# Performance work log

Measured on AMD Instinct MI355X. Metric: run time of the kernel, lower is better.

Reference implementation:

```python
import jax, jax.numpy as jnp
import numpy as np

EPS = 1e-5
SLOPE = 0.01  # torch LeakyReLU default negative slope


def _bn(h, gamma, beta):
    # BatchNorm1d in training mode: biased batch statistics over the batch dim
    mu = jnp.mean(h, axis=0)
    var = jnp.var(h, axis=0)
    return gamma * (h - mu) * jax.lax.rsqrt(var + EPS) + beta


def _leaky(h):
    return jnp.where(h >= 0, h, SLOPE * h)


def _forward(x, adj, w_gc1, b_gc1, w_gc2, b_gc2, w_gc3, b_gc3,
             w_fc0, b_fc0, g_fc0, be_fc0, w_fc1, b_fc1, g_fc1, be_fc1, w_fc2, b_fc2):
    B, S, Fp1 = x.shape
    F = Fp1 - 1
    N = adj.shape[0]
    # --- scatter: build per-sample node features from first S-1 timesteps ---
    sids = x[:, :S - 1, -2].astype(jnp.int32)                                   # [B,S-1]
    feats = jnp.concatenate([x[:, :S - 1, :-2], x[:, :S - 1, -1:]], axis=-1)    # [B,S-1,F]
    X = jnp.zeros((B, N, F), x.dtype).at[jnp.arange(B)[:, None], sids].set(feats)
    # --- symmetric-normalized adjacency with self loops: D^-1/2 (A+I) D^-1/2 ---
    A = adj + jnp.eye(N, dtype=adj.dtype)
    d = jax.lax.rsqrt(jnp.sum(A, axis=1))
    Ahat = d[:, None] * A * d[None, :]                                          # [N,N]
    # --- fc0 branch on last-timestep features ---
    h0 = _leaky(_bn(x[:, -1, :-2] @ w_fc0 + b_fc0, g_fc0, be_fc0))              # [B,FH]
    # --- 3-layer GCN: relu(Ahat @ X @ W + b) ---
    X = jax.nn.relu(jnp.einsum('mn,bnf->bmf', Ahat, X) @ w_gc1 + b_gc1)
    X = jax.nn.relu(jnp.einsum('mn,bnf->bmf', Ahat, X) @ w_gc2 + b_gc2)
    X = jax.nn.relu(jnp.einsum('mn,bnf->bmf', Ahat, X) @ w_gc3 + b_gc3)         # [B,N,GH]
    # --- gather station-specific rows ---
    sid_last = x[:, -1, -2].astype(jnp.int32)                                   # [B]
    g = X[jnp.arange(B), sid_last]                                              # [B,GH]
    # --- fusion MLP head ---
    h = jnp.concatenate([h0, g], axis=1)
    h = _leaky(_bn(h @ w_fc1 + b_fc1, g_fc1, be_fc1))
    return jax.nn.sigmoid(h @ w_fc2 + b_fc2)                                    # [B,1]


def setup_inputs() -> dict:
    B, N, S, F = 128, 2000, 64, 16
    GH, FH = 512, 512
    key = jax.random.key(0)
    ks = jax.random.split(key, 12)
    x = jax.random.normal(ks[0], (B, S, F + 1), dtype=jnp.float32)
    # station-id column (-2): unique ids per sample so scatter writes are unambiguous
    perms = jax.vmap(lambda k: jax.random.permutation(k, N)[:S])(jax.random.split(ks[1], B))  # [B,S]
    x = x.at[:, :, -2].set(perms.astype(jnp.float32))
    # random symmetric 0/1 adjacency, avg degree ~32
    adj = (jax.random.uniform(ks[2], (N, N)) < (32.0 / N)).astype(jnp.float32)
    adj = jnp.maximum(adj, adj.T)

    def lin(k, i, o):
        kw, kb = jax.random.split(k)
        bound = 1.0 / np.sqrt(i)
        w = jax.random.uniform(kw, (i, o), jnp.float32, -bound, bound)
        b = jax.random.uniform(kb, (o,), jnp.float32, -bound, bound)
        return w, b

    w_gc1, b_gc1 = lin(ks[3], F, GH // 2)
    w_gc2, b_gc2 = lin(ks[4], GH // 2, GH // 2)
    w_gc3, b_gc3 = lin(ks[5], GH // 2, GH)
    w_fc0, b_fc0 = lin(ks[6], F - 1, FH)
    w_fc1, b_fc1 = lin(ks[7], GH + FH, FH)
    w_fc2, b_fc2 = lin(ks[8], FH, 1)
    g_fc0 = jnp.ones((FH,), jnp.float32)
    be_fc0 = jnp.zeros((FH,), jnp.float32)
    g_fc1 = jnp.ones((FH,), jnp.float32)
    be_fc1 = jnp.zeros((FH,), jnp.float32)
    return dict(x=x, adj=adj, w_gc1=w_gc1, b_gc1=b_gc1, w_gc2=w_gc2, b_gc2=b_gc2,
                w_gc3=w_gc3, b_gc3=b_gc3, w_fc0=w_fc0, b_fc0=b_fc0, g_fc0=g_fc0, be_fc0=be_fc0,
                w_fc1=w_fc1, b_fc1=b_fc1, g_fc1=g_fc1, be_fc1=be_fc1, w_fc2=w_fc2, b_fc2=b_fc2)


def reference(x, adj, w_gc1, b_gc1, w_gc2, b_gc2, w_gc3, b_gc3, w_fc0, b_fc0, g_fc0, be_fc0,
              w_fc1, b_fc1, g_fc1, be_fc1, w_fc2, b_fc2):
    return _forward(x, adj, w_gc1, b_gc1, w_gc2, b_gc2, w_gc3, b_gc3,
                    w_fc0, b_fc0, g_fc0, be_fc0, w_fc1, b_fc1, g_fc1, be_fc1, w_fc2, b_fc2)
```

## Files before the change

kernel.cpp:

```cpp
#include <hip/hip_runtime.h>
#include <hip/hip_bf16.h>

typedef __hip_bfloat16 bf16;
typedef short s8v __attribute__((ext_vector_type(8)));
typedef float f4v __attribute__((ext_vector_type(4)));
typedef float f2v __attribute__((ext_vector_type(2)));

#define B   128
#define N   2000
#define S   64
#define CAP 128
#define JT  16
#define JG  8
#define XROW 1088

__device__ inline ushort bfb(float v) {
    union { __hip_bfloat16 h; ushort u; } c; c.h = __float2bfloat16(v); return c.u;
}

__global__ __launch_bounds__(256) void k_prep0(const float* __restrict__ adj,
                                               float* __restrict__ d,
                                               const float* __restrict__ w1,
                                               const float* __restrict__ w2,
                                               uint4* __restrict__ wf1,
                                               uint4* __restrict__ wf2) {
    int blk = blockIdx.x;
    if (blk < N) {
        int m = blk;
        const float* row = adj + (size_t)m * N;
        float s = 0.f;
        for (int c = threadIdx.x; c < N; c += 256) s += row[c];
        for (int o = 32; o > 0; o >>= 1) s += __shfl_down(s, o);
        __shared__ float red[4];
        int wave = threadIdx.x >> 6;
        if ((threadIdx.x & 63) == 0) red[wave] = s;
        __syncthreads();
        if (threadIdx.x == 0)
            d[m] = rsqrtf(red[0] + red[1] + red[2] + red[3] + 1.0f);
    } else {
        int blk2 = blk - N;
        if (blk2 < 4) {
            int e = blk2 * 256 + threadIdx.x;
            int ct = e >> 6, l = e & 63;
            int kg = l >> 4, ch = ct * 16 + (l & 15);
            ushort h[8];
#pragma unroll
            for (int j = 0; j < 8; ++j) {
                int f = kg * 8 + j;
                h[j] = (f < 16) ? bfb(w1[f * 256 + ch]) : (ushort)0;
            }
            uint4 r;
            r.x = h[0] | ((uint)h[1] << 16);
            r.y = h[2] | ((uint)h[3] << 16);
            r.z = h[4] | ((uint)h[5] << 16);
            r.w = h[6] | ((uint)h[7] << 16);
            wf1[e] = r;
        } else {
            int e = (blk2 - 4) * 256 + threadIdx.x;
            int l = e & 63;
            int kc = (e >> 6) & 7;
            int nt = e >> 9;
            int col = l & 15, kg = l >> 4;
            ushort h[8];
#pragma unroll
            for (int i = 0; i < 8; ++i) {
                int k = kc * 32 + kg * 8 + i;
                h[i] = bfb(w2[k * 256 + nt * 16 + col]);
            }
            uint4 r;
            r.x = h[0] | ((uint)h[1] << 16);
            r.y = h[2] | ((uint)h[3] << 16);
            r.z = h[4] | ((uint)h[5] << 16);
            r.w = h[6] | ((uint)h[7] << 16);
            wf2[e] = r;
        }
    }
}

__global__ __launch_bounds__(256) void k_prep1(const float* __restrict__ adj,
                                               const float* __restrict__ d,
                                               const float* __restrict__ x,
                                               int* __restrict__ cnt,
                                               int* __restrict__ idx,
                                               float* __restrict__ val,
                                               int* __restrict__ sid,
                                               int* __restrict__ sid_last,
                                               uint4* __restrict__ feA) {
    int blk = blockIdx.x;
    if (blk < 500) {
        int m = blk * 4 + (threadIdx.x >> 6);
        int lane = threadIdx.x & 63;
        const float* row = adj + (size_t)m * N;
        float dm = d[m];
        int base = 0;
        for (int c0 = 0; c0 < N; c0 += 64) {
            int c = c0 + lane;
            float a = 0.f;
            if (c < N) { a = row[c]; if (c == m) a += 1.0f; }
            bool pred = (a != 0.f);
            unsigned long long mask = __ballot(pred);
            int pos = base + __popcll(mask & ((1ull << lane) - 1ull));
            if (pred && pos < CAP) {
                idx[m * CAP + pos] = c;
                val[m * CAP + pos] = dm * d[c] * a;
            }
            base += (int)__popcll(mask);
        }
        if (lane == 0) cnt[m] = base < CAP ? base : CAP;
    } else {
        int b = blk - 500, tid = threadIdx.x;
        const float* xb = x + (size_t)b * XROW;
        __shared__ float dss_sh[63];
        __shared__ float fe_sh[64][16];
        if (tid < S - 1) {
            int s_ = (int)xb[tid * 17 + 15];
            sid[b * (S - 1) + tid] = s_;
            dss_sh[tid] = d[s_];
        }
        if (tid == S - 1) sid_last[b] = (int)xb[(S - 1) * 17 + 15];
        if (tid >= 240 && tid < 256) fe_sh[63][tid - 240] = 0.f;
        __syncthreads();
        for (int i = tid; i < (S - 1) * 16; i += 256) {
            int t = i >> 4, f = i & 15;
            fe_sh[t][f] = dss_sh[t] * xb[t * 17 + (f < 15 ? f : 16)];
        }
        __syncthreads();
        if (tid < 128) {
            int kc = tid >> 6, l = tid & 63;
            int f = l & 15, tg = l >> 4;
            ushort h[8];
#pragma unroll
            for (int j = 0; j < 8; ++j)
                h[j] = bfb(fe_sh[kc * 32 + tg * 8 + j][f]);
            uint4 r;
            r.x = h[0] | ((uint)h[1] << 16);
            r.y = h[2] | ((uint)h[3] << 16);
            r.z = h[4] | ((uint)h[5] << 16);
            r.w = h[6] | ((uint)h[7] << 16);
            feA[(b * 2 + kc) * 64 + l] = r;
        }
    }
}

__global__ __launch_bounds__(256) void k_x1(const float* __restrict__ adj,
                                            const float* __restrict__ d,
                                            const int* __restrict__ sid,
                                            const uint4* __restrict__ feA,
                                            const uint4* __restrict__ wfrag,
                                            const float* __restrict__ b1,
                                            unsigned char* __restrict__ X1) {
    __shared__ int sv[64];
    __shared__ __align__(16) ushort Ylds[64][40];
    __shared__ float b1s[256];
    __shared__ __align__(16) uint Xs[4][16][68];
    int b = blockIdx.y, p0 = blockIdx.x * 64, tid = threadIdx.x;
    b1s[tid] = b1[tid];
    if (tid < 63) sv[tid] = sid[b * 63 + tid];
    if (tid == 63) sv[63] = 0;
    __syncthreads();

    int l = tid & 63, wv = tid >> 6;
    int lm = l & 15, lg = l >> 4;
    int pt = p0 + wv * 16;
    int pcol = pt + lm;
    bool pv = (pcol < N);
    int pc = pv ? pcol : 0;

    s8v a1_0 = *(const s8v*)&feA[(b * 2 + 0) * 64 + l];
    s8v a1_1 = *(const s8v*)&feA[(b * 2 + 1) * 64 + l];

    int ss[16];
#pragma unroll
    for (int q = 0; q < 16; ++q)
        ss[q] = sv[(q >> 3) * 32 + lg * 8 + (q & 7)];
    float av[16];
#pragma unroll
    for (int q = 0; q < 16; ++q)
        av[q] = adj[(size_t)ss[q] * N + pc];
#pragma unroll
    for (int q = 0; q < 16; ++q) {
        av[q] = pv ? av[q] : 0.f;
        if (pcol == ss[q]) av[q] += 1.0f;
    }
    ushort h[16];
#pragma unroll
    for (int q = 0; q < 16; ++q) h[q] = bfb(av[q]);
    s8v b1f, b2f;
    {
        uint4 t0, t1;
        t0.x = h[0] | ((uint)h[1] << 16);  t0.y = h[2] | ((uint)h[3] << 16);
        t0.z = h[4] | ((uint)h[5] << 16);  t0.w = h[6] | ((uint)h[7] << 16);
        t1.x = h[8] | ((uint)h[9] << 16);  t1.y = h[10] | ((uint)h[11] << 16);
        t1.z = h[12] | ((uint)h[13] << 16); t1.w = h[14] | ((uint)h[15] << 16);
        b1f = *(s8v*)&t0; b2f = *(s8v*)&t1;
    }
    f4v D1 = (f4v){0.f, 0.f, 0.f, 0.f};
    D1 = __builtin_amdgcn_mfma_f32_16x16x32_bf16(a1_0, b1f, D1, 0, 0, 0);
    D1 = __builtin_amdgcn_mfma_f32_16x16x32_bf16(a1_1, b2f, D1, 0, 0, 0);
    float dp = d[pc] * (pv ? 1.f : 0.f);
    uint2 pk;
    pk.x = bfb(D1[0] * dp) | ((uint)bfb(D1[1] * dp) << 16);
    pk.y = bfb(D1[2] * dp) | ((uint)bfb(D1[3] * dp) << 16);
    *(uint2*)&Ylds[wv * 16 + lm][lg * 4] = pk;
    *(uint2*)&Ylds[wv * 16 + lm][16 + lg * 4] = make_uint2(0u, 0u);
    __syncthreads();

    s8v yf = *(const s8v*)&Ylds[wv * 16 + lm][lg * 8];
    f4v acc2[16];
#pragma unroll
    for (int ct = 0; ct < 16; ++ct) acc2[ct] = (f4v){0.f, 0.f, 0.f, 0.f};
#pragma unroll
    for (int ct = 0; ct < 16; ++ct) {
        s8v wfv = *(const s8v*)&wfrag[ct * 64 + l];
        acc2[ct] = __builtin_amdgcn_mfma_f32_16x16x32_bf16(wfv, yf, acc2[ct], 0, 0, 0);
    }
#pragma unroll
    for (int ct = 0; ct < 16; ++ct) {
        float4 bz = *(float4*)&b1s[ct * 16 + lg * 4];
        float v0 = acc2[ct][0] + bz.x; v0 = v0 > 0.f ? v0 : 0.f;
        float v1 = acc2[ct][1] + bz.y; v1 = v1 > 0.f ? v1 : 0.f;
        float v2 = acc2[ct][2] + bz.z; v2 = v2 > 0.f ? v2 : 0.f;
        float v3 = acc2[ct][3] + bz.w; v3 = v3 > 0.f ? v3 : 0.f;
        uint pk8 = (uint)__builtin_amdgcn_cvt_pk_fp8_f32(v0, v1, 0, false);
        pk8 = (uint)__builtin_amdgcn_cvt_pk_fp8_f32(v2, v3, (int)pk8, true);
        Xs[wv][lm][ct * 4 + lg] = pk8;
    }
    __syncthreads();
    {
        uint4* dstb = (uint4*)((uint*)X1 + ((size_t)b * N + p0 + wv * 16) * 64);
#pragma unroll
        for (int i = 0; i < 4; ++i) {
            int g = l + 64 * i;
            int r = g >> 4, c4 = g & 15;
            if (p0 + wv * 16 + r < N)
                dstb[g] = *(uint4*)&Xs[wv][r][c4 * 4];
        }
    }
}

__global__ __launch_bounds__(256) void k_gather(const int* __restrict__ cnt,
                                                const int* __restrict__ idxA,
                                                const float* __restrict__ valA,
                                                const int* __restrict__ sid_last,
                                                const unsigned char* __restrict__ X1,
                                                bf16* __restrict__ aggG) {
    __shared__ int   nns[JG];
    __shared__ int   ncn_s[JG];
    __shared__ int   nidx[JG][CAP];
    __shared__ float nval[JG][CAP];
    int b = blockIdx.y, j0 = blockIdx.x * JG, tid = threadIdx.x;
    int m = sid_last[b];
    int cj = cnt[m];
    if (tid < JG) {
        int j = j0 + tid;
        int n = idxA[m * CAP + (j < cj ? j : 0)];
        nns[tid] = n;
        ncn_s[tid] = (j < cj) ? cnt[n] : 0;
    }
    __syncthreads();
    for (int i = tid; i < JG * CAP; i += 256) {
        int jj = i >> 7, k = i & (CAP - 1);
        int n = nns[jj], c = ncn_s[jj];
        nidx[jj][k] = (k < c) ? idxA[n * CAP + k] : 0;
        nval[jj][k] = (k < c) ? valA[n * CAP + k] : 0.f;
    }
    __syncthreads();
    int lane = tid & 63;
    int w = __builtin_amdgcn_readfirstlane(tid >> 6);
    int la = w * 2, lb = la + 1;
    const uint* X1bl = (const uint*)X1 + (size_t)b * N * 64 + lane;
    int cA = ncn_s[la], cB = ncn_s[lb];
    int cmax = cA > cB ? cA : cB;
    float aA0 = 0.f, aA1 = 0.f, aA2 = 0.f, aA3 = 0.f;
    float aB0 = 0.f, aB1 = 0.f, aB2 = 0.f, aB3 = 0.f;
    if (cmax > 0) {
        uint uA0 = X1bl[(size_t)nidx[la][0] * 64]; float vA0 = nval[la][0];
        uint uA1 = X1bl[(size_t)nidx[la][1] * 64]; float vA1 = nval[la][1];
        uint uB0 = X1bl[(size_t)nidx[lb][0] * 64]; float vB0 = nval[lb][0];
        uint uB1 = X1bl[(size_t)nidx[lb][1] * 64]; float vB1 = nval[lb][1];
        int c2 = (cmax + 1) & ~1;
        for (int k = 0; k < c2; k += 2) {
            int k2 = k + 2; k2 = k2 < CAP ? k2 : CAP - 1;
            int k3 = k + 3; k3 = k3 < CAP ? k3 : CAP - 1;
            uint cA0 = uA0, cA1 = uA1, cB0 = uB0, cB1 = uB1;
            float wA0 = vA0, wA1 = vA1, wB0 = vB0, wB1 = vB1;
            uA0 = X1bl[(size_t)nidx[la][k2] * 64]; vA0 = nval[la][k2];
            uA1 = X1bl[(size_t)nidx[la][k3] * 64]; vA1 = nval[la][k3];
            uB0 = X1bl[(size_t)nidx[lb][k2] * 64]; vB0 = nval[lb][k2];
            uB1 = X1bl[(size_t)nidx[lb][k3] * 64]; vB1 = nval[lb][k3];
            f2v lo, hi;
            lo = __builtin_amdgcn_cvt_pk_f32_fp8((int)cA0, false);
            hi = __builtin_amdgcn_cvt_pk_f32_fp8((int)cA0, true);
            aA0 += wA0 * lo.x; aA1 += wA0 * lo.y; aA2 += wA0 * hi.x; aA3 += wA0 * hi.y;
            lo = __builtin_amdgcn_cvt_pk_f32_fp8((int)cA1, false);
            hi = __builtin_amdgcn_cvt_pk_f32_fp8((int)cA1, true);
            aA0 += wA1 * lo.x; aA1 += wA1 * lo.y; aA2 += wA1 * hi.x; aA3 += wA1 * hi.y;
            lo = __builtin_amdgcn_cvt_pk_f32_fp8((int)cB0, false);
            hi = __builtin_amdgcn_cvt_pk_f32_fp8((int)cB0, true);
            aB0 += wB0 * lo.x; aB1 += wB0 * lo.y; aB2 += wB0 * hi.x; aB3 += wB0 * hi.y;
            lo = __builtin_amdgcn_cvt_pk_f32_fp8((int)cB1, false);
            hi = __builtin_amdgcn_cvt_pk_f32_fp8((int)cB1, true);
            aB0 += wB1 * lo.x; aB1 += wB1 * lo.y; aB2 += wB1 * hi.x; aB3 += wB1 * hi.y;
        }
    }
    uint2 pkA, pkB;
    pkA.x = bfb(aA0) | ((uint)bfb(aA1) << 16);
    pkA.y = bfb(aA2) | ((uint)bfb(aA3) << 16);
    pkB.x = bfb(aB0) | ((uint)bfb(aB1) << 16);
    pkB.y = bfb(aB2) | ((uint)bfb(aB3) << 16);
    uint2* ag = (uint2*)aggG;
    ag[((size_t)b * CAP + j0 + la) * 64 + lane] = pkA;
    ag[((size_t)b * CAP + j0 + lb) * 64 + lane] = pkB;
}

__global__ __launch_bounds__(256) void k_x2mm(const int* __restrict__ cnt,
                                              const int* __restrict__ sid_last,
                                              const bf16* __restrict__ aggG,
                                              const uint4* __restrict__ w2f,
                                              const float* __restrict__ b2,
                                              float* __restrict__ X2) {
    __shared__ ushort agg[JT][264];
    int b = blockIdx.y, j0 = blockIdx.x * JT, tid = threadIdx.x;
    int m = sid_last[b];
    int cj = cnt[m];
    if (j0 >= cj) return;
    int nj = cj - j0; if (nj > JT) nj = JT;
    {
        const uint4* src = (const uint4*)(aggG + ((size_t)b * CAP + j0) * 256);
        for (int i = tid; i < 512; i += 256) {
            int row = i >> 5, col = i & 31;
            *(uint4*)&agg[row][col * 8] = src[i];
        }
    }
    __syncthreads();
    int lane = tid & 63;
    int w = __builtin_amdgcn_readfirstlane(tid >> 6);
    int col = lane & 15, rg = lane >> 4;
    s8v af[8];
#pragma unroll
    for (int kc = 0; kc < 8; ++kc)
        af[kc] = *(const s8v*)&agg[col][kc * 32 + rg * 8];
#pragma unroll
    for (int t = 0; t < 4; ++t) {
        int nt = w * 4 + t;
        f4v acc = (f4v){0.f, 0.f, 0.f, 0.f};
#pragma unroll
        for (int kc = 0; kc < 8; ++kc) {
            s8v bf = *(const s8v*)&w2f[(nt * 8 + kc) * 64 + lane];
            acc = __builtin_amdgcn_mfma_f32_16x16x32_bf16(af[kc], bf, acc, 0, 0, 0);
        }
        float bv = b2[nt * 16 + col];
        float* dst = X2 + ((size_t)b * CAP + j0) * 256 + nt * 16 + col;
#pragma unroll
        for (int i = 0; i < 4; ++i) {
            int row = rg * 4 + i;
            if (row < nj) {
                float vv = acc[i] + bv;
                dst[(size_t)row * 256] = vv > 0.f ? vv : 0.f;
            }
        }
    }
}

__global__ __launch_bounds__(256) void k_gagg(const int* __restrict__ cnt,
                                              const float* __restrict__ valA,
                                              const int* __restrict__ sid_last,
                                              const float* __restrict__ X2,
                                              float* __restrict__ gaggP) {
    int b = blockIdx.x, q = blockIdx.y, tid = threadIdx.x;
    int m = sid_last[b];
    int cj = cnt[m];
    int jlo = q * 32, jhi = jlo + 32 < cj ? jlo + 32 : cj;
    const float* vp = valA + m * CAP;
    const float* xp = X2 + (size_t)b * CAP * 256 + tid;
    float a0 = 0.f, a1 = 0.f, a2 = 0.f, a3 = 0.f;
    int jj = jlo;
    for (; jj + 4 <= jhi; jj += 4) {
        a0 += vp[jj]     * xp[(size_t)(jj)     * 256];
        a1 += vp[jj + 1] * xp[(size_t)(jj + 1) * 256];
        a2 += vp[jj + 2] * xp[(size_t)(jj + 2) * 256];
        a3 += vp[jj + 3] * xp[(size_t)(jj + 3) * 256];
    }
    for (; jj < jhi; ++jj) a0 += vp[jj] * xp[(size_t)jj * 256];
    gaggP[((size_t)b * 4 + q) * 256 + tid] = (a0 + a1) + (a2 + a3);
}

__global__ __launch_bounds__(256) void k_gmm(const float* __restrict__ gaggP,
                                             const float* __restrict__ w3,
                                             const float* __restrict__ b3,
                                             float* __restrict__ g) {
    int b = blockIdx.x, ot = blockIdx.y, tid = threadIdx.x;
    __shared__ float h[256];
    {
        const float* p = gaggP + (size_t)b * 4 * 256 + tid;
        h[tid] = p[0] + p[256] + p[512] + p[768];
    }
    __syncthreads();
    int q  = tid & 31;
    int kg = tid >> 5;
    const float4* w4 = (const float4*)w3;
    int wq = ot * 32 + q;
    float4 acc = {0.f, 0.f, 0.f, 0.f};
    for (int k = kg * 32; k < kg * 32 + 32; ++k) {
        float hk = h[k];
        float4 w = w4[(size_t)k * 128 + wq];
        acc.x += hk * w.x; acc.y += hk * w.y; acc.z += hk * w.z; acc.w += hk * w.w;
    }
    __shared__ float4 red[8][32];
    red[kg][q] = acc;
    __syncthreads();
    if (tid < 32) {
        float4 s = red[0][tid];
#pragma unroll
        for (int gr = 1; gr < 8; ++gr) {
            float4 r = red[gr][tid];
            s.x += r.x; s.y += r.y; s.z += r.z; s.w += r.w;
        }
        int ob = ot * 128 + tid * 4;
        s.x += b3[ob];     s.x = s.x > 0.f ? s.x : 0.f;
        s.y += b3[ob + 1]; s.y = s.y > 0.f ? s.y : 0.f;
        s.z += b3[ob + 2]; s.z = s.z > 0.f ? s.z : 0.f;
        s.w += b3[ob + 3]; s.w = s.w > 0.f ? s.w : 0.f;
        *(float4*)&g[(size_t)b * 512 + ob] = s;
    }
}

__global__ __launch_bounds__(256) void k_fc0s(const float* __restrict__ x,
                                              const float* __restrict__ w0,
                                              const float* __restrict__ b0,
                                              float* __restrict__ hp0,
                                              float* __restrict__ mu0,
                                              float* __restrict__ rstd0) {
    int tid = threadIdx.x;
    int c = tid >> 7, b = tid & 127;
    int o = blockIdx.x * 2 + c;
    const float* xr = x + (size_t)b * XROW + (S - 1) * 17;
    float acc = b0[o];
#pragma unroll
    for (int f = 0; f < 15; ++f) acc += xr[f] * w0[f * 512 + o];
    hp0[b * 512 + o] = acc;
    float s = acc, s2 = acc * acc;
    for (int off = 32; off > 0; off >>= 1) {
        s += __shfl_down(s, off);
        s2 += __shfl_down(s2, off);
    }
    __shared__ float rs[4], rs2[4];
    int wv = tid >> 6;
    if ((tid & 63) == 0) { rs[wv] = s; rs2[wv] = s2; }
    __syncthreads();
    if ((tid & 127) == 0) {
        float S1 = rs[c * 2] + rs[c * 2 + 1];
        float S2 = rs2[c * 2] + rs2[c * 2 + 1];
        float m = S1 * (1.f / B);
        float var = S2 * (1.f / B) - m * m;
        mu0[o] = m;
        rstd0[o] = rsqrtf(var + 1e-5f);
    }
}

__global__ __launch_bounds__(256) void k_bn1w(const float* __restrict__ h,
                                              float* __restrict__ mu,
                                              float* __restrict__ rstd) {
    int tid = threadIdx.x;
    int o = blockIdx.x * 32 + (tid & 31);
    int bg = tid >> 5;
    float s = 0.f, s2 = 0.f;
    for (int b = bg * 16; b < bg * 16 + 16; ++b) {
        float v = h[b * 512 + o];
        s += v; s2 += v * v;
    }
    __shared__ float rs[8][32], rs2[8][32];
    rs[bg][tid & 31] = s; rs2[bg][tid & 31] = s2;
    __syncthreads();
    if (tid < 32) {
        float S1 = 0.f, S2 = 0.f;
#pragma unroll
        for (int g2 = 0; g2 < 8; ++g2) { S1 += rs[g2][tid]; S2 += rs2[g2][tid]; }
        float m = S1 * (1.f / B);
        float var = S2 * (1.f / B) - m * m;
        mu[blockIdx.x * 32 + tid] = m;
        rstd[blockIdx.x * 32 + tid] = rsqrtf(var + 1e-5f);
    }
}

__global__ __launch_bounds__(256) void k_fc1(const float* __restrict__ hp0,
                                             const float* __restrict__ mu0,
                                             const float* __restrict__ rstd0,
                                             const float* __restrict__ gam,
                                             const float* __restrict__ bet,
                                             const float* __restrict__ gbuf,
                                             const float* __restrict__ w1,
                                             const float* __restrict__ b1,
                                             float* __restrict__ hp1) {
    int b = blockIdx.x, ot = blockIdx.y, tid = threadIdx.x;
    __shared__ float h[1024];
    for (int o = tid; o < 512; o += 256) {
        float v = hp0[b * 512 + o];
        v = gam[o] * (v - mu0[o]) * rstd0[o] + bet[o];
        h[o] = v >= 0.f ? v : 0.01f * v;
        h[512 + o] = gbuf[(size_t)b * 512 + o];
    }
    __syncthreads();
    int q  = tid & 31;
    int kg = tid >> 5;
    const float4* w4 = (const float4*)w1;
    int wq = ot * 32 + q;
    float4 acc = {0.f, 0.f, 0.f, 0.f};
    for (int k = kg * 128; k < kg * 128 + 128; ++k) {
        float hk = h[k];
        float4 w = w4[(size_t)k * 128 + wq];
        acc.x += hk * w.x; acc.y += hk * w.y; acc.z += hk * w.z; acc.w += hk * w.w;
    }
    __shared__ float4 red[8][32];
    red[kg][q] = acc;
    __syncthreads();
    if (tid < 32) {
        float4 s = red[0][tid];
#pragma unroll
        for (int gr = 1; gr < 8; ++gr) {
            float4 r = red[gr][tid];
            s.x += r.x; s.y += r.y; s.z += r.z; s.w += r.w;
        }
        int ob = ot * 128 + tid * 4;
        s.x += b1[ob]; s.y += b1[ob + 1]; s.z += b1[ob + 2]; s.w += b1[ob + 3];
        *(float4*)&hp1[b * 512 + ob] = s;
    }
}

__global__ __launch_bounds__(64) void k_out(const float* __restrict__ hp1,
                                            const float* __restrict__ mu1,
                                            const float* __restrict__ rstd1,
                                            const float* __restrict__ gam,
                                            const float* __restrict__ bet,
                                            const float* __restrict__ w2,
                                            const float* __restrict__ b2,
                                            float* __restrict__ out) {
    int b = blockIdx.x, lane = threadIdx.x;
    float acc = 0.f;
    for (int o = lane; o < 512; o += 64) {
        float v = hp1[b * 512 + o];
        v = gam[o] * (v - mu1[o]) * rstd1[o] + bet[o];
        v = v >= 0.f ? v : 0.01f * v;
        acc += v * w2[o];
    }
    for (int off = 32; off > 0; off >>= 1) acc += __shfl_down(acc, off);
    if (lane == 0) out[b] = 1.f / (1.f + expf(-(acc + b2[0])));
}

static inline size_t align256(size_t x) { return (x + 255) & ~(size_t)255; }

extern "C" void kernel_launch(void* const* d_in, const int* in_sizes, int n_in,
                              void* d_out, int out_size, void* d_ws, size_t ws_size,
                              hipStream_t stream) {
    const float* x     = (const float*)d_in[0];
    const float* adj   = (const float*)d_in[1];
    const float* w_gc1 = (const float*)d_in[2];
    const float* b_gc1 = (const float*)d_in[3];
    const float* w_gc2 = (const float*)d_in[4];
    const float* b_gc2 = (const float*)d_in[5];
    const float* w_gc3 = (const float*)d_in[6];
    const float* b_gc3 = (const float*)d_in[7];
    const float* w_fc0 = (const float*)d_in[8];
    const float* b_fc0 = (const float*)d_in[9];
    const float* g_fc0 = (const float*)d_in[10];
    const float* be_fc0= (const float*)d_in[11];
    const float* w_fc1 = (const float*)d_in[12];
    const float* b_fc1 = (const float*)d_in[13];
    const float* g_fc1 = (const float*)d_in[14];
    const float* be_fc1= (const float*)d_in[15];
    const float* w_fc2 = (const float*)d_in[16];
    const float* b_fc2 = (const float*)d_in[17];

    char* wsp = (char*)d_ws;
    size_t off = 0;
    auto alloc = [&](size_t bytes) { void* p = wsp + off; off = align256(off + bytes); return p; };
    float* d_deg   = (float*)alloc((size_t)N * 4);
    int*   sid     = (int*)  alloc((size_t)B * 63 * 4);
    int*   sidl    = (int*)  alloc((size_t)B * 4);
    uint4* feA     = (uint4*)alloc((size_t)B * 2 * 64 * 16);
    uint4* wfrag   = (uint4*)alloc((size_t)1024 * 16);
    uint4* w2frag  = (uint4*)alloc((size_t)8192 * 16);
    int*   csr_cnt = (int*)  alloc((size_t)N * 4);
    int*   csr_idx = (int*)  alloc((size_t)N * CAP * 4);
    float* csr_val = (float*)alloc((size_t)N * CAP * 4);
    unsigned char* X1 = (unsigned char*)alloc((size_t)B * N * 256);
    bf16*  aggG    = (bf16*) alloc((size_t)B * CAP * 256 * 2);
    float* X2      = (float*)alloc((size_t)B * CAP * 256 * 4);
    float* gaggP   = (float*)alloc((size_t)B * 4 * 256 * 4);
    float* gbuf    = (float*)alloc((size_t)B * 512 * 4);
    float* hp0     = (float*)alloc((size_t)B * 512 * 4);
    float* mu0     = (float*)alloc(512 * 4);
    float* rstd0   = (float*)alloc(512 * 4);
    float* hp1     = (float*)alloc((size_t)B * 512 * 4);
    float* mu1     = (float*)alloc(512 * 4);
    float* rstd1   = (float*)alloc(512 * 4);

    k_prep0 <<<N + 36, 256, 0, stream>>>(adj, d_deg, w_gc1, w_gc2, wfrag, w2frag);
    k_prep1 <<<500 + B, 256, 0, stream>>>(adj, d_deg, x, csr_cnt, csr_idx, csr_val, sid, sidl, feA);
    k_x1    <<<dim3(32, B), 256, 0, stream>>>(adj, d_deg, sid, feA, wfrag, b_gc1, X1);
    k_gather<<<dim3(CAP / JG, B), 256, 0, stream>>>(csr_cnt, csr_idx, csr_val, sidl, X1, aggG);
    k_x2mm  <<<dim3(CAP / JT, B), 256, 0, stream>>>(csr_cnt, sidl, aggG, w2frag, b_gc2, X2);
    k_gagg  <<<dim3(B, 4), 256, 0, stream>>>(csr_cnt, csr_val, sidl, X2, gaggP);
    k_gmm   <<<dim3(B, 4), 256, 0, stream>>>(gaggP, w_gc3, b_gc3, gbuf);
    k_fc0s  <<<256, 256, 0, stream>>>(x, w_fc0, b_fc0, hp0, mu0, rstd0);
    k_fc1   <<<dim3(B, 4), 256, 0, stream>>>(hp0, mu0, rstd0, g_fc0, be_fc0, gbuf, w_fc1, b_fc1, hp1);
    k_bn1w  <<<16, 256, 0, stream>>>(hp1, mu1, rstd1);
    k_out   <<<B, 64, 0, stream>>>(hp1, mu1, rstd1, g_fc1, be_fc1, w_fc2, b_fc2, (float*)d_out);
}
```

Baseline: 134.7 us.

## Fuse layer-2 GEMM with weighted aggregation and deepen gather prefetch

The layer-2 MFMA kernel now applies bias and ReLU, then directly reduces its rows weighted by the adjacency values into per-tile partial sums. This removes the X2 intermediate write/read and the separate k_gagg launch. k_gmm sums up to 8 partials per sample based on the neighbor count. Separately, the gather loop is unrolled to 4 neighbors per step with 4-deep prefetch, adding more loads in flight at the cost of extra registers.

```diff
diff --git a/kernel.cpp b/kernel.cpp
--- a/kernel.cpp
+++ b/kernel.cpp
@@ -274,20 +274,34 @@
     float aA0 = 0.f, aA1 = 0.f, aA2 = 0.f, aA3 = 0.f;
     float aB0 = 0.f, aB1 = 0.f, aB2 = 0.f, aB3 = 0.f;
     if (cmax > 0) {
-        uint uA0 = X1bl[(size_t)nidx[la][0] * 64]; float vA0 = nval[la][0];
-        uint uA1 = X1bl[(size_t)nidx[la][1] * 64]; float vA1 = nval[la][1];
-        uint uB0 = X1bl[(size_t)nidx[lb][0] * 64]; float vB0 = nval[lb][0];
-        uint uB1 = X1bl[(size_t)nidx[lb][1] * 64]; float vB1 = nval[lb][1];
-        int c2 = (cmax + 1) & ~1;
-        for (int k = 0; k < c2; k += 2) {
-            int k2 = k + 2; k2 = k2 < CAP ? k2 : CAP - 1;
-            int k3 = k + 3; k3 = k3 < CAP ? k3 : CAP - 1;
-            uint cA0 = uA0, cA1 = uA1, cB0 = uB0, cB1 = uB1;
-            float wA0 = vA0, wA1 = vA1, wB0 = vB0, wB1 = vB1;
-            uA0 = X1bl[(size_t)nidx[la][k2] * 64]; vA0 = nval[la][k2];
-            uA1 = X1bl[(size_t)nidx[la][k3] * 64]; vA1 = nval[la][k3];
-            uB0 = X1bl[(size_t)nidx[lb][k2] * 64]; vB0 = nval[lb][k2];
-            uB1 = X1bl[(size_t)nidx[lb][k3] * 64]; vB1 = nval[lb][k3];
+        uint uA0, uA1, uA2, uA3, uB0, uB1, uB2, uB3;
+        float vA0, vA1, vA2, vA3, vB0, vB1, vB2, vB3;
+        uA0 = X1bl[(size_t)nidx[la][0] * 64]; vA0 = nval[la][0];
+        uA1 = X1bl[(size_t)nidx[la][1] * 64]; vA1 = nval[la][1];
+        uA2 = X1bl[(size_t)nidx[la][2] * 64]; vA2 = nval[la][2];
+        uA3 = X1bl[(size_t)nidx[la][3] * 64]; vA3 = nval[la][3];
+        uB0 = X1bl[(size_t)nidx[lb][0] * 64]; vB0 = nval[lb][0];
+        uB1 = X1bl[(size_t)nidx[lb][1] * 64]; vB1 = nval[lb][1];
+        uB2 = X1bl[(size_t)nidx[lb][2] * 64]; vB2 = nval[lb][2];
+        uB3 = X1bl[(size_t)nidx[lb][3] * 64]; vB3 = nval[lb][3];
+        int c4 = (cmax + 3) & ~3;
+        for (int k = 0; k < c4; k += 4) {
+            uint cA0 = uA0, cA1 = uA1, cA2 = uA2, cA3 = uA3;
+            uint cB0 = uB0, cB1 = uB1, cB2 = uB2, cB3 = uB3;
+            float wA0 = vA0, wA1 = vA1, wA2 = vA2, wA3 = vA3;
+            float wB0 = vB0, wB1 = vB1, wB2 = vB2, wB3 = vB3;
+            int k4 = k + 4; k4 = k4 < CAP ? k4 : CAP - 1;
+            int k5 = k + 5; k5 = k5 < CAP ? k5 : CAP - 1;
+            int k6 = k + 6; k6 = k6 < CAP ? k6 : CAP - 1;
+            int k7 = k + 7; k7 = k7 < CAP ? k7 : CAP - 1;
+            uA0 = X1bl[(size_t)nidx[la][k4] * 64]; vA0 = nval[la][k4];
+            uA1 = X1bl[(size_t)nidx[la][k5] * 64]; vA1 = nval[la][k5];
+            uA2 = X1bl[(size_t)nidx[la][k6] * 64]; vA2 = nval[la][k6];
+            uA3 = X1bl[(size_t)nidx[la][k7] * 64]; vA3 = nval[la][k7];
+            uB0 = X1bl[(size_t)nidx[lb][k4] * 64]; vB0 = nval[lb][k4];
+            uB1 = X1bl[(size_t)nidx[lb][k5] * 64]; vB1 = nval[lb][k5];
+            uB2 = X1bl[(size_t)nidx[lb][k6] * 64]; vB2 = nval[lb][k6];
+            uB3 = X1bl[(size_t)nidx[lb][k7] * 64]; vB3 = nval[lb][k7];
             f2v lo, hi;
             lo = __builtin_amdgcn_cvt_pk_f32_fp8((int)cA0, false);
             hi = __builtin_amdgcn_cvt_pk_f32_fp8((int)cA0, true);
@@ -295,12 +309,24 @@
             lo = __builtin_amdgcn_cvt_pk_f32_fp8((int)cA1, false);
             hi = __builtin_amdgcn_cvt_pk_f32_fp8((int)cA1, true);
             aA0 += wA1 * lo.x; aA1 += wA1 * lo.y; aA2 += wA1 * hi.x; aA3 += wA1 * hi.y;
+            lo = __builtin_amdgcn_cvt_pk_f32_fp8((int)cA2, false);
+            hi = __builtin_amdgcn_cvt_pk_f32_fp8((int)cA2, true);
+            aA0 += wA2 * lo.x; aA1 += wA2 * lo.y; aA2 += wA2 * hi.x; aA3 += wA2 * hi.y;
+            lo = __builtin_amdgcn_cvt_pk_f32_fp8((int)cA3, false);
+            hi = __builtin_amdgcn_cvt_pk_f32_fp8((int)cA3, true);
+            aA0 += wA3 * lo.x; aA1 += wA3 * lo.y; aA2 += wA3 * hi.x; aA3 += wA3 * hi.y;
             lo = __builtin_amdgcn_cvt_pk_f32_fp8((int)cB0, false);
             hi = __builtin_amdgcn_cvt_pk_f32_fp8((int)cB0, true);
             aB0 += wB0 * lo.x; aB1 += wB0 * lo.y; aB2 += wB0 * hi.x; aB3 += wB0 * hi.y;
             lo = __builtin_amdgcn_cvt_pk_f32_fp8((int)cB1, false);
             hi = __builtin_amdgcn_cvt_pk_f32_fp8((int)cB1, true);
             aB0 += wB1 * lo.x; aB1 += wB1 * lo.y; aB2 += wB1 * hi.x; aB3 += wB1 * hi.y;
+            lo = __builtin_amdgcn_cvt_pk_f32_fp8((int)cB2, false);
+            hi = __builtin_amdgcn_cvt_pk_f32_fp8((int)cB2, true);
+            aB0 += wB2 * lo.x; aB1 += wB2 * lo.y; aB2 += wB2 * hi.x; aB3 += wB2 * hi.y;
+            lo = __builtin_amdgcn_cvt_pk_f32_fp8((int)cB3, false);
+            hi = __builtin_amdgcn_cvt_pk_f32_fp8((int)cB3, true);
+            aB0 += wB3 * lo.x; aB1 += wB3 * lo.y; aB2 += wB3 * hi.x; aB3 += wB3 * hi.y;
         }
     }
     uint2 pkA, pkB;
@@ -313,18 +339,21 @@
     ag[((size_t)b * CAP + j0 + lb) * 64 + lane] = pkB;
 }
 
-__global__ __launch_bounds__(256) void k_x2mm(const int* __restrict__ cnt,
-                                              const int* __restrict__ sid_last,
-                                              const bf16* __restrict__ aggG,
-                                              const uint4* __restrict__ w2f,
-                                              const float* __restrict__ b2,
-                                              float* __restrict__ X2) {
+__global__ __launch_bounds__(256) void k_x2g(const int* __restrict__ cnt,
+                                             const int* __restrict__ sid_last,
+                                             const float* __restrict__ valA,
+                                             const bf16* __restrict__ aggG,
+                                             const uint4* __restrict__ w2f,
+                                             const float* __restrict__ b2,
+                                             float* __restrict__ gaggP) {
     __shared__ ushort agg[JT][264];
+    __shared__ float vs[JT];
     int b = blockIdx.y, j0 = blockIdx.x * JT, tid = threadIdx.x;
     int m = sid_last[b];
     int cj = cnt[m];
     if (j0 >= cj) return;
     int nj = cj - j0; if (nj > JT) nj = JT;
+    if (tid < JT) vs[tid] = (tid < nj) ? valA[m * CAP + j0 + tid] : 0.f;
     {
         const uint4* src = (const uint4*)(aggG + ((size_t)b * CAP + j0) * 256);
         for (int i = tid; i < 512; i += 256) {
@@ -340,6 +369,7 @@
 #pragma unroll
     for (int kc = 0; kc < 8; ++kc)
         af[kc] = *(const s8v*)&agg[col][kc * 32 + rg * 8];
+    float* outp = gaggP + ((size_t)b * 8 + blockIdx.x) * 256;
 #pragma unroll
     for (int t = 0; t < 4; ++t) {
         int nt = w * 4 + t;
@@ -350,50 +380,35 @@
             acc = __builtin_amdgcn_mfma_f32_16x16x32_bf16(af[kc], bf, acc, 0, 0, 0);
         }
         float bv = b2[nt * 16 + col];
-        float* dst = X2 + ((size_t)b * CAP + j0) * 256 + nt * 16 + col;
+        float p = 0.f;
 #pragma unroll
         for (int i = 0; i < 4; ++i) {
-            int row = rg * 4 + i;
-            if (row < nj) {
-                float vv = acc[i] + bv;
-                dst[(size_t)row * 256] = vv > 0.f ? vv : 0.f;
-            }
-        }
-    }
-}
-
-__global__ __launch_bounds__(256) void k_gagg(const int* __restrict__ cnt,
-                                              const float* __restrict__ valA,
-                                              const int* __restrict__ sid_last,
-                                              const float* __restrict__ X2,
-                                              float* __restrict__ gaggP) {
-    int b = blockIdx.x, q = blockIdx.y, tid = threadIdx.x;
-    int m = sid_last[b];
-    int cj = cnt[m];
-    int jlo = q * 32, jhi = jlo + 32 < cj ? jlo + 32 : cj;
-    const float* vp = valA + m * CAP;
-    const float* xp = X2 + (size_t)b * CAP * 256 + tid;
-    float a0 = 0.f, a1 = 0.f, a2 = 0.f, a3 = 0.f;
-    int jj = jlo;
-    for (; jj + 4 <= jhi; jj += 4) {
-        a0 += vp[jj]     * xp[(size_t)(jj)     * 256];
-        a1 += vp[jj + 1] * xp[(size_t)(jj + 1) * 256];
-        a2 += vp[jj + 2] * xp[(size_t)(jj + 2) * 256];
-        a3 += vp[jj + 3] * xp[(size_t)(jj + 3) * 256];
-    }
-    for (; jj < jhi; ++jj) a0 += vp[jj] * xp[(size_t)jj * 256];
-    gaggP[((size_t)b * 4 + q) * 256 + tid] = (a0 + a1) + (a2 + a3);
-}
-
-__global__ __launch_bounds__(256) void k_gmm(const float* __restrict__ gaggP,
+            float vv = acc[i] + bv;
+            vv = vv > 0.f ? vv : 0.f;
+            p += vs[rg * 4 + i] * vv;
+        }
+        p += __shfl_xor(p, 16);
+        p += __shfl_xor(p, 32);
+        if (lane < 16) outp[nt * 16 + col] = p;
+    }
+}
+
+__global__ __launch_bounds__(256) void k_gmm(const int* __restrict__ cnt,
+                                             const int* __restrict__ sid_last,
+                                             const float* __restrict__ gaggP,
                                              const float* __restrict__ w3,
                                              const float* __restrict__ b3,
                                              float* __restrict__ g) {
     int b = blockIdx.x, ot = blockIdx.y, tid = threadIdx.x;
     __shared__ float h[256];
     {
-        const float* p = gaggP + (size_t)b * 4 * 256 + tid;
-        h[tid] = p[0] + p[256] + p[512] + p[768];
+        int m = sid_last[b];
+        int cj = cnt[m];
+        int nq = (cj + JT - 1) / JT;
+        const float* p = gaggP + (size_t)b * 8 * 256 + tid;
+        float s = 0.f;
+        for (int q = 0; q < nq; ++q) s += p[q * 256];
+        h[tid] = s;
     }
     __syncthreads();
     int q  = tid & 31;
@@ -585,8 +600,7 @@
     float* csr_val = (float*)alloc((size_t)N * CAP * 4);
     unsigned char* X1 = (unsigned char*)alloc((size_t)B * N * 256);
     bf16*  aggG    = (bf16*) alloc((size_t)B * CAP * 256 * 2);
-    float* X2      = (float*)alloc((size_t)B * CAP * 256 * 4);
-    float* gaggP   = (float*)alloc((size_t)B * 4 * 256 * 4);
+    float* gaggP   = (float*)alloc((size_t)B * 8 * 256 * 4);
     float* gbuf    = (float*)alloc((size_t)B * 512 * 4);
     float* hp0     = (float*)alloc((size_t)B * 512 * 4);
     float* mu0     = (float*)alloc(512 * 4);
@@ -599,9 +613,8 @@
     k_prep1 <<<500 + B, 256, 0, stream>>>(adj, d_deg, x, csr_cnt, csr_idx, csr_val, sid, sidl, feA);
     k_x1    <<<dim3(32, B), 256, 0, stream>>>(adj, d_deg, sid, feA, wfrag, b_gc1, X1);
     k_gather<<<dim3(CAP / JG, B), 256, 0, stream>>>(csr_cnt, csr_idx, csr_val, sidl, X1, aggG);
-    k_x2mm  <<<dim3(CAP / JT, B), 256, 0, stream>>>(csr_cnt, sidl, aggG, w2frag, b_gc2, X2);
-    k_gagg  <<<dim3(B, 4), 256, 0, stream>>>(csr_cnt, csr_val, sidl, X2, gaggP);
-    k_gmm   <<<dim3(B, 4), 256, 0, stream>>>(gaggP, w_gc3, b_gc3, gbuf);
+    k_x2g   <<<dim3(CAP / JT, B), 256, 0, stream>>>(csr_cnt, sidl, csr_val, aggG, w2frag, b_gc2, gaggP);
+    k_gmm   <<<dim3(B, 4), 256, 0, stream>>>(csr_cnt, sidl, gaggP, w_gc3, b_gc3, gbuf);
     k_fc0s  <<<256, 256, 0, stream>>>(x, w_fc0, b_fc0, hp0, mu0, rstd0);
     k_fc1   <<<dim3(B, 4), 256, 0, stream>>>(hp0, mu0, rstd0, g_fc0, be_fc0, gbuf, w_fc1, b_fc1, hp1);
     k_bn1w  <<<16, 256, 0, stream>>>(hp1, mu1, rstd1);
```

New measurement: 124.7 us. 7.4% less time.
